# Kernel tuning notes

Hardware: AMD Instinct MI355X
Metric: run time of the kernel (lower is better)

Reference implementation:

```python
import jax, jax.numpy as jnp
import numpy as np

IMG_H, IMG_W = 432.0, 768.0
B, N = 8, 1_000_000


def setup_inputs() -> dict:
    key = jax.random.key(0)
    k1, k2 = jax.random.split(key)
    scores = jax.random.uniform(k1, (B, N, 1), dtype=jnp.float32)
    # center-format boxes (x, y, w, h) roughly in image coords so masks fire
    scale = jnp.array([IMG_W, IMG_H, 256.0, 256.0], dtype=jnp.float32)
    rps = jax.random.uniform(k2, (B, N, 4), dtype=jnp.float32) * scale
    return {"scores": scores, "rps": rps, "n_train_pre_nms": 12000}


def _anchors_clip(boxes):
    # boxes: [B, N, 4] in (cx, cy, w, h)
    cx, cy, w, h = boxes[..., 0], boxes[..., 1], boxes[..., 2], boxes[..., 3]
    x1 = jnp.clip(cx - w * 0.5, 0.0, IMG_W)
    x2 = jnp.clip(cx + w * 0.5, 0.0, IMG_W)
    y1 = jnp.clip(cy - h * 0.5, 0.0, IMG_H)
    y2 = jnp.clip(cy + h * 0.5, 0.0, IMG_H)
    nw = x2 - x1
    nh = y2 - y1
    nx = x1 + nw * 0.5
    ny = y1 + nh * 0.5
    return jnp.stack([nx, ny, nw, nh], axis=-1)


def reference(scores, rps, n_train_pre_nms):
    rois = _anchors_clip(rps)                                   # [B, N, 4]
    mask = ((rois[..., 2] > 16.0) & (rois[..., 3] > 16.0))
    s = scores * mask.astype(scores.dtype)[..., None]           # [B, N, 1]
    # full descending argsort along anchor dim, keep top n_train_pre_nms
    order = jnp.argsort(-s[..., 0], axis=1)[:, :n_train_pre_nms]  # [B, K]
    rois_sel = jnp.take_along_axis(rois, order[..., None], axis=1)  # [B, K, 4]
    s_sel = jnp.take_along_axis(s, order[..., None], axis=1)        # [B, K, 1]
    return rois_sel, s_sel
```

## Files before the change

### kernel.cpp

```cpp
#include <hip/hip_runtime.h>
#include <stdint.h>

#define BATCH   8
#define NITEMS  1000000
#define NB      4096
#define NBLK    64
#define CAP     32768
#define IMG_W   768.0f
#define IMG_H   432.0f

static __device__ __forceinline__ float clip0(float v, float hi) {
    return fminf(fmaxf(v, 0.0f), hi);
}

__global__ void k_zero(unsigned* __restrict__ ctrA,
                       unsigned* __restrict__ ctrB,
                       unsigned* __restrict__ meta) {
    int idx = blockIdx.x * blockDim.x + threadIdx.x;
    int total = BATCH * NB;
    for (int i = idx; i < total; i += gridDim.x * blockDim.x) {
        ctrA[i] = 0u;
        ctrB[i] = 0u;
    }
    if (idx < BATCH * 4) meta[idx] = 0u;
}

__global__ __launch_bounds__(512)
void k_bits_hist(const float* __restrict__ scores,
                 const float4* __restrict__ rps,
                 unsigned* __restrict__ bits_arr,
                 unsigned* __restrict__ partial) {
    __shared__ unsigned h[NB];
    const int b = blockIdx.y, blk = blockIdx.x, tid = threadIdx.x;
    for (int k = tid; k < NB; k += 512) h[k] = 0u;
    __syncthreads();
    const int base = b * NITEMS;
    for (int i = blk * 512 + tid; i < NITEMS; i += NBLK * 512) {
        float4 box = rps[base + i];
        float s = scores[base + i];
        float x1 = clip0(box.x - box.z * 0.5f, IMG_W);
        float x2 = clip0(box.x + box.z * 0.5f, IMG_W);
        float y1 = clip0(box.y - box.w * 0.5f, IMG_H);
        float y2 = clip0(box.y + box.w * 0.5f, IMG_H);
        float nw = x2 - x1, nh = y2 - y1;
        bool m = (nw > 16.0f) && (nh > 16.0f);
        unsigned bits = __float_as_uint(m ? s : 0.0f);
        bits_arr[base + i] = bits;
        if (bits) atomicAdd(&h[bits >> 20], 1u);
    }
    __syncthreads();
    unsigned* dst = partial + ((size_t)(b * NBLK + blk)) * NB;
    for (int k = tid; k < NB; k += 512) dst[k] = h[k];
}

__global__ __launch_bounds__(512)
void k_fine_hist(const unsigned* __restrict__ bits_arr,
                 const unsigned* __restrict__ meta,
                 unsigned* __restrict__ partial) {
    __shared__ unsigned h[NB];
    const int b = blockIdx.y, blk = blockIdx.x, tid = threadIdx.x;
    const unsigned cbb = meta[b * 4 + 0];
    for (int k = tid; k < NB; k += 512) h[k] = 0u;
    __syncthreads();
    const int base = b * NITEMS;
    for (int i = blk * 512 + tid; i < NITEMS; i += NBLK * 512) {
        unsigned bits = bits_arr[base + i];
        if (bits && (bits >> 20) == cbb) atomicAdd(&h[(bits >> 8) & 0xFFF], 1u);
    }
    __syncthreads();
    unsigned* dst = partial + ((size_t)(b * NBLK + blk)) * NB;
    for (int k = tid; k < NB; k += 512) dst[k] = h[k];
}

__global__ __launch_bounds__(256)
void k_reduce(const unsigned* __restrict__ partial,
              unsigned* __restrict__ hist) {
    const int b = blockIdx.y;
    const int g = blockIdx.x * 256 + threadIdx.x;
    const unsigned* p = partial + (size_t)b * NBLK * NB + g;
    unsigned s = 0;
    for (int k = 0; k < NBLK; k++) s += p[(size_t)k * NB];
    hist[b * NB + g] = s;
}

__global__ __launch_bounds__(1024)
void k_scan(const unsigned* __restrict__ hist,
            unsigned* __restrict__ suffix,
            unsigned* __restrict__ meta,
            int K, int mode) {
    const int b = blockIdx.x, tid = threadIdx.x;
    __shared__ unsigned lh[NB];
    __shared__ unsigned sc[1024];
    const unsigned* h = hist + b * NB;
    for (int k = tid; k < NB; k += 1024) lh[k] = h[k];
    __syncthreads();
    unsigned c[4], p[4];
    unsigned run = 0;
    for (int k = 0; k < 4; k++) {
        int r = tid * 4 + k;
        c[k] = lh[NB - 1 - r];
        run += c[k];
        p[k] = run;
    }
    sc[tid] = run;
    __syncthreads();
    unsigned x = run;
    for (int off = 1; off < 1024; off <<= 1) {
        unsigned t = (tid >= off) ? sc[tid - off] : 0u;
        __syncthreads();
        x += t;
        sc[tid] = x;
        __syncthreads();
    }
    unsigned exclBase = x - run;
    unsigned off0 = mode ? meta[b * 4 + 1] : 0u;
    for (int k = 0; k < 4; k++) {
        int r = tid * 4 + k;
        int g = NB - 1 - r;
        unsigned excl = exclBase + p[k] - c[k];
        suffix[b * NB + g] = excl;
        unsigned tot = off0 + excl;
        if (tot < (unsigned)K && tot + c[k] >= (unsigned)K) {
            if (mode == 0) {
                meta[b * 4 + 0] = (unsigned)g;
                meta[b * 4 + 1] = excl;
            } else {
                meta[b * 4 + 2] = (unsigned)g;
                meta[b * 4 + 3] = tot + c[k];
            }
        }
    }
}

__global__ __launch_bounds__(512)
void k_compact(const unsigned* __restrict__ bits_arr,
               const unsigned* __restrict__ meta,
               const unsigned* __restrict__ csuf,
               const unsigned* __restrict__ fsuf,
               unsigned* __restrict__ ctrA,
               unsigned* __restrict__ ctrB,
               unsigned long long* __restrict__ cand) {
    const int b = blockIdx.y;
    const unsigned cbb = meta[b * 4 + 0];
    const unsigned nAbove = meta[b * 4 + 1];
    const unsigned fb = meta[b * 4 + 2];
    const int base = b * NITEMS;
    for (int i = blockIdx.x * 512 + threadIdx.x; i < NITEMS; i += NBLK * 512) {
        unsigned bits = bits_arr[base + i];
        if (!bits) continue;
        unsigned cb = bits >> 20;
        if (cb < cbb) continue;
        unsigned slot;
        if (cb > cbb) {
            slot = csuf[b * NB + cb] + atomicAdd(&ctrA[b * NB + cb], 1u);
        } else {
            unsigned f = (bits >> 8) & 0xFFF;
            if (f < fb) continue;
            slot = nAbove + fsuf[b * NB + f] + atomicAdd(&ctrB[b * NB + f], 1u);
        }
        if (slot < CAP)
            cand[(size_t)b * CAP + slot] =
                ((unsigned long long)bits << 32) | (unsigned)(~(unsigned)i);
    }
}

__global__ __launch_bounds__(256)
void k_rank_out(const unsigned long long* __restrict__ cand,
                const unsigned* __restrict__ meta,
                const unsigned* __restrict__ csuf,
                const unsigned* __restrict__ chist,
                const unsigned* __restrict__ fsuf,
                const unsigned* __restrict__ fhist,
                const float4* __restrict__ rps,
                float* __restrict__ out,
                int K) {
    const int b = blockIdx.y;
    unsigned total = meta[b * 4 + 3];
    if (total > CAP) total = CAP;
    const unsigned p = blockIdx.x * 256 + threadIdx.x;
    if (p >= total) return;
    const unsigned long long key = cand[(size_t)b * CAP + p];
    const unsigned bits = (unsigned)(key >> 32);
    const unsigned cb = bits >> 20;
    const unsigned cbb = meta[b * 4 + 0];
    const unsigned nAbove = meta[b * 4 + 1];
    unsigned sbase, scnt;
    if (cb > cbb) {
        sbase = csuf[b * NB + cb];
        scnt  = chist[b * NB + cb];
    } else {
        unsigned f = (bits >> 8) & 0xFFF;
        sbase = nAbove + fsuf[b * NB + f];
        scnt  = fhist[b * NB + f];
    }
    unsigned send = sbase + scnt;
    if (send > total) send = total;
    unsigned rank = sbase;
    for (unsigned j = sbase; j < send; j++)
        rank += (cand[(size_t)b * CAP + j] > key) ? 1u : 0u;
    if (rank < (unsigned)K) {
        unsigned idx = ~((unsigned)key);
        float s = __uint_as_float(bits);
        float4 box = rps[(size_t)b * NITEMS + idx];
        float x1 = clip0(box.x - box.z * 0.5f, IMG_W);
        float x2 = clip0(box.x + box.z * 0.5f, IMG_W);
        float y1 = clip0(box.y - box.w * 0.5f, IMG_H);
        float y2 = clip0(box.y + box.w * 0.5f, IMG_H);
        float nw = x2 - x1, nh = y2 - y1;
        float nx = x1 + nw * 0.5f, ny = y1 + nh * 0.5f;
        ((float4*)out)[(size_t)b * K + rank] = make_float4(nx, ny, nw, nh);
        out[(size_t)BATCH * K * 4 + (size_t)b * K + rank] = s;
    }
}

extern "C" void kernel_launch(void* const* d_in, const int* in_sizes, int n_in,
                              void* d_out, int out_size, void* d_ws, size_t ws_size,
                              hipStream_t stream) {
    const float*  scores = (const float*)d_in[0];
    const float4* rps    = (const float4*)d_in[1];
    const int K = out_size / (BATCH * 5);

    uint8_t* w = (uint8_t*)d_ws;
    unsigned* bits_arr = (unsigned*)(w);
    unsigned* partial  = (unsigned*)(w + 32000000);
    unsigned* chist    = (unsigned*)(w + 40400000);
    unsigned* csuf     = (unsigned*)(w + 40600000);
    unsigned* fhist    = (unsigned*)(w + 40800000);
    unsigned* fsuf     = (unsigned*)(w + 41000000);
    unsigned* ctrA     = (unsigned*)(w + 41200000);
    unsigned* ctrB     = (unsigned*)(w + 41400000);
    unsigned* meta     = (unsigned*)(w + 41600000);
    unsigned long long* cand = (unsigned long long*)(w + 41700000);

    k_zero<<<dim3(256), dim3(256), 0, stream>>>(ctrA, ctrB, meta);
    k_bits_hist<<<dim3(NBLK, BATCH), dim3(512), 0, stream>>>(scores, rps, bits_arr, partial);
    k_reduce<<<dim3(NB / 256, BATCH), dim3(256), 0, stream>>>(partial, chist);
    k_scan<<<dim3(BATCH), dim3(1024), 0, stream>>>(chist, csuf, meta, K, 0);
    k_fine_hist<<<dim3(NBLK, BATCH), dim3(512), 0, stream>>>(bits_arr, meta, partial);
    k_reduce<<<dim3(NB / 256, BATCH), dim3(256), 0, stream>>>(partial, fhist);
    k_scan<<<dim3(BATCH), dim3(1024), 0, stream>>>(fhist, fsuf, meta, K, 1);
    k_compact<<<dim3(NBLK, BATCH), dim3(512), 0, stream>>>(bits_arr, meta, csuf, fsuf,
                                                           ctrA, ctrB, cand);
    k_rank_out<<<dim3(CAP / 256, BATCH), dim3(256), 0, stream>>>(cand, meta, csuf, chist,
                                                                 fsuf, fhist, rps,
                                                                 (float*)d_out, K);
}
```

Baseline: 103.7 us.

## Replace two-pass exponent radix select with single value-binned histogram pass

```diff
diff --git a/kernel.cpp b/kernel.cpp
--- a/kernel.cpp
+++ b/kernel.cpp
@@ -4,7 +4,7 @@
 #define BATCH   8
 #define NITEMS  1000000
 #define NB      4096
-#define NBLK    64
+#define NBLK    128
 #define CAP     32768
 #define IMG_W   768.0f
 #define IMG_H   432.0f
@@ -13,15 +13,18 @@
     return fminf(fmaxf(v, 0.0f), hi);
 }
 
-__global__ void k_zero(unsigned* __restrict__ ctrA,
-                       unsigned* __restrict__ ctrB,
+static __device__ __forceinline__ unsigned val_bin(float s) {
+    int b = (int)(s * (float)NB);
+    if (b > NB - 1) b = NB - 1;
+    if (b < 0) b = 0;
+    return (unsigned)b;
+}
+
+__global__ void k_zero(unsigned* __restrict__ ctr,
                        unsigned* __restrict__ meta) {
     int idx = blockIdx.x * blockDim.x + threadIdx.x;
     int total = BATCH * NB;
-    for (int i = idx; i < total; i += gridDim.x * blockDim.x) {
-        ctrA[i] = 0u;
-        ctrB[i] = 0u;
-    }
+    for (int i = idx; i < total; i += gridDim.x * blockDim.x) ctr[i] = 0u;
     if (idx < BATCH * 4) meta[idx] = 0u;
 }
 
@@ -29,7 +32,7 @@
 void k_bits_hist(const float* __restrict__ scores,
                  const float4* __restrict__ rps,
                  unsigned* __restrict__ bits_arr,
-                 unsigned* __restrict__ partial) {
+                 unsigned short* __restrict__ partial) {
     __shared__ unsigned h[NB];
     const int b = blockIdx.y, blk = blockIdx.x, tid = threadIdx.x;
     for (int k = tid; k < NB; k += 512) h[k] = 0u;
@@ -44,40 +47,22 @@
         float y2 = clip0(box.y + box.w * 0.5f, IMG_H);
         float nw = x2 - x1, nh = y2 - y1;
         bool m = (nw > 16.0f) && (nh > 16.0f);
-        unsigned bits = __float_as_uint(m ? s : 0.0f);
+        float sm = m ? s : 0.0f;
+        unsigned bits = __float_as_uint(sm);
         bits_arr[base + i] = bits;
-        if (bits) atomicAdd(&h[bits >> 20], 1u);
+        if (bits) atomicAdd(&h[val_bin(sm)], 1u);
     }
     __syncthreads();
-    unsigned* dst = partial + ((size_t)(b * NBLK + blk)) * NB;
-    for (int k = tid; k < NB; k += 512) dst[k] = h[k];
-}
-
-__global__ __launch_bounds__(512)
-void k_fine_hist(const unsigned* __restrict__ bits_arr,
-                 const unsigned* __restrict__ meta,
-                 unsigned* __restrict__ partial) {
-    __shared__ unsigned h[NB];
-    const int b = blockIdx.y, blk = blockIdx.x, tid = threadIdx.x;
-    const unsigned cbb = meta[b * 4 + 0];
-    for (int k = tid; k < NB; k += 512) h[k] = 0u;
-    __syncthreads();
-    const int base = b * NITEMS;
-    for (int i = blk * 512 + tid; i < NITEMS; i += NBLK * 512) {
-        unsigned bits = bits_arr[base + i];
-        if (bits && (bits >> 20) == cbb) atomicAdd(&h[(bits >> 8) & 0xFFF], 1u);
-    }
-    __syncthreads();
-    unsigned* dst = partial + ((size_t)(b * NBLK + blk)) * NB;
-    for (int k = tid; k < NB; k += 512) dst[k] = h[k];
+    unsigned short* dst = partial + ((size_t)(b * NBLK + blk)) * NB;
+    for (int k = tid; k < NB; k += 512) dst[k] = (unsigned short)h[k];
 }
 
 __global__ __launch_bounds__(256)
-void k_reduce(const unsigned* __restrict__ partial,
+void k_reduce(const unsigned short* __restrict__ partial,
               unsigned* __restrict__ hist) {
     const int b = blockIdx.y;
     const int g = blockIdx.x * 256 + threadIdx.x;
-    const unsigned* p = partial + (size_t)b * NBLK * NB + g;
+    const unsigned short* p = partial + (size_t)b * NBLK * NB + g;
     unsigned s = 0;
     for (int k = 0; k < NBLK; k++) s += p[(size_t)k * NB];
     hist[b * NB + g] = s;
@@ -87,7 +72,7 @@
 void k_scan(const unsigned* __restrict__ hist,
             unsigned* __restrict__ suffix,
             unsigned* __restrict__ meta,
-            int K, int mode) {
+            int K) {
     const int b = blockIdx.x, tid = threadIdx.x;
     __shared__ unsigned lh[NB];
     __shared__ unsigned sc[1024];
@@ -113,21 +98,15 @@
         __syncthreads();
     }
     unsigned exclBase = x - run;
-    unsigned off0 = mode ? meta[b * 4 + 1] : 0u;
     for (int k = 0; k < 4; k++) {
         int r = tid * 4 + k;
         int g = NB - 1 - r;
         unsigned excl = exclBase + p[k] - c[k];
         suffix[b * NB + g] = excl;
-        unsigned tot = off0 + excl;
-        if (tot < (unsigned)K && tot + c[k] >= (unsigned)K) {
-            if (mode == 0) {
-                meta[b * 4 + 0] = (unsigned)g;
-                meta[b * 4 + 1] = excl;
-            } else {
-                meta[b * 4 + 2] = (unsigned)g;
-                meta[b * 4 + 3] = tot + c[k];
-            }
+        if (excl < (unsigned)K && excl + c[k] >= (unsigned)K) {
+            meta[b * 4 + 0] = (unsigned)g;
+            meta[b * 4 + 1] = excl;
+            meta[b * 4 + 3] = excl + c[k];
         }
     }
 }
@@ -136,28 +115,17 @@
 void k_compact(const unsigned* __restrict__ bits_arr,
                const unsigned* __restrict__ meta,
                const unsigned* __restrict__ csuf,
-               const unsigned* __restrict__ fsuf,
-               unsigned* __restrict__ ctrA,
-               unsigned* __restrict__ ctrB,
+               unsigned* __restrict__ ctr,
                unsigned long long* __restrict__ cand) {
     const int b = blockIdx.y;
     const unsigned cbb = meta[b * 4 + 0];
-    const unsigned nAbove = meta[b * 4 + 1];
-    const unsigned fb = meta[b * 4 + 2];
     const int base = b * NITEMS;
     for (int i = blockIdx.x * 512 + threadIdx.x; i < NITEMS; i += NBLK * 512) {
         unsigned bits = bits_arr[base + i];
         if (!bits) continue;
-        unsigned cb = bits >> 20;
-        if (cb < cbb) continue;
-        unsigned slot;
-        if (cb > cbb) {
-            slot = csuf[b * NB + cb] + atomicAdd(&ctrA[b * NB + cb], 1u);
-        } else {
-            unsigned f = (bits >> 8) & 0xFFF;
-            if (f < fb) continue;
-            slot = nAbove + fsuf[b * NB + f] + atomicAdd(&ctrB[b * NB + f], 1u);
-        }
+        unsigned g = val_bin(__uint_as_float(bits));
+        if (g < cbb) continue;
+        unsigned slot = csuf[b * NB + g] + atomicAdd(&ctr[b * NB + g], 1u);
         if (slot < CAP)
             cand[(size_t)b * CAP + slot] =
                 ((unsigned long long)bits << 32) | (unsigned)(~(unsigned)i);
@@ -169,8 +137,6 @@
                 const unsigned* __restrict__ meta,
                 const unsigned* __restrict__ csuf,
                 const unsigned* __restrict__ chist,
-                const unsigned* __restrict__ fsuf,
-                const unsigned* __restrict__ fhist,
                 const float4* __restrict__ rps,
                 float* __restrict__ out,
                 int K) {
@@ -181,19 +147,9 @@
     if (p >= total) return;
     const unsigned long long key = cand[(size_t)b * CAP + p];
     const unsigned bits = (unsigned)(key >> 32);
-    const unsigned cb = bits >> 20;
-    const unsigned cbb = meta[b * 4 + 0];
-    const unsigned nAbove = meta[b * 4 + 1];
-    unsigned sbase, scnt;
-    if (cb > cbb) {
-        sbase = csuf[b * NB + cb];
-        scnt  = chist[b * NB + cb];
-    } else {
-        unsigned f = (bits >> 8) & 0xFFF;
-        sbase = nAbove + fsuf[b * NB + f];
-        scnt  = fhist[b * NB + f];
-    }
-    unsigned send = sbase + scnt;
+    const unsigned g = val_bin(__uint_as_float(bits));
+    unsigned sbase = csuf[b * NB + g];
+    unsigned send = sbase + chist[b * NB + g];
     if (send > total) send = total;
     unsigned rank = sbase;
     for (unsigned j = sbase; j < send; j++)
@@ -221,27 +177,19 @@
     const int K = out_size / (BATCH * 5);
 
     uint8_t* w = (uint8_t*)d_ws;
-    unsigned* bits_arr = (unsigned*)(w);
-    unsigned* partial  = (unsigned*)(w + 32000000);
-    unsigned* chist    = (unsigned*)(w + 40400000);
-    unsigned* csuf     = (unsigned*)(w + 40600000);
-    unsigned* fhist    = (unsigned*)(w + 40800000);
-    unsigned* fsuf     = (unsigned*)(w + 41000000);
-    unsigned* ctrA     = (unsigned*)(w + 41200000);
-    unsigned* ctrB     = (unsigned*)(w + 41400000);
-    unsigned* meta     = (unsigned*)(w + 41600000);
-    unsigned long long* cand = (unsigned long long*)(w + 41700000);
+    unsigned* bits_arr        = (unsigned*)(w);
+    unsigned short* partial   = (unsigned short*)(w + 32000000);
+    unsigned* chist           = (unsigned*)(w + 40500000);
+    unsigned* csuf            = (unsigned*)(w + 40700000);
+    unsigned* ctr             = (unsigned*)(w + 40900000);
+    unsigned* meta            = (unsigned*)(w + 41100000);
+    unsigned long long* cand  = (unsigned long long*)(w + 41200000);
 
-    k_zero<<<dim3(256), dim3(256), 0, stream>>>(ctrA, ctrB, meta);
+    k_zero<<<dim3(256), dim3(256), 0, stream>>>(ctr, meta);
     k_bits_hist<<<dim3(NBLK, BATCH), dim3(512), 0, stream>>>(scores, rps, bits_arr, partial);
     k_reduce<<<dim3(NB / 256, BATCH), dim3(256), 0, stream>>>(partial, chist);
-    k_scan<<<dim3(BATCH), dim3(1024), 0, stream>>>(chist, csuf, meta, K, 0);
-    k_fine_hist<<<dim3(NBLK, BATCH), dim3(512), 0, stream>>>(bits_arr, meta, partial);
-    k_reduce<<<dim3(NB / 256, BATCH), dim3(256), 0, stream>>>(partial, fhist);
-    k_scan<<<dim3(BATCH), dim3(1024), 0, stream>>>(fhist, fsuf, meta, K, 1);
-    k_compact<<<dim3(NBLK, BATCH), dim3(512), 0, stream>>>(bits_arr, meta, csuf, fsuf,
-                                                           ctrA, ctrB, cand);
+    k_scan<<<dim3(BATCH), dim3(1024), 0, stream>>>(chist, csuf, meta, K);
+    k_compact<<<dim3(NBLK, BATCH), dim3(512), 0, stream>>>(bits_arr, meta, csuf, ctr, cand);
     k_rank_out<<<dim3(CAP / 256, BATCH), dim3(256), 0, stream>>>(cand, meta, csuf, chist,
-                                                                 fsuf, fhist, rps,
-                                                                 (float*)d_out, K);
+                                                                 rps, (float*)d_out, K);
 }
```

Measured after the change: 148.6 us. +43.3%, slower.
